# Kernel optimization log

Hardware: AMD Instinct MI355X
Metric: run time of the kernel (lower is better)

The kernel has to match this reference:

```python
import jax, jax.numpy as jnp
import numpy as np

# --- dims (match init_kwargs) ---
VOCAB = 16; D_MODEL = 512; NLAYERS = 4; LMAX = 1024; NCLASSES = 2
D_STATE = 128; D_CONV = 4; EXPAND = 2; HEADDIM = 64; PAD_IDX = 4
D_INNER = EXPAND * D_MODEL            # 1024
NHEADS = D_INNER // HEADDIM           # 16
CONV_DIM = D_INNER + 2 * D_STATE      # 1280 (ngroups=1)
D_IN_PROJ = 2 * D_INNER + 2 * D_STATE + NHEADS  # 2320
BATCH = 8; SEQ = 1024
EPS = 1e-5


def silu(x):
    return x * jax.nn.sigmoid(x)


def setup_inputs() -> dict:
    key = jax.random.key(0)
    ks = jax.random.split(key, 24)
    s = 0.02
    emb = jax.random.normal(ks[0], (VOCAB, D_MODEL), jnp.float32) * s
    emb = emb.at[PAD_IDX].set(0.0)  # padding_idx row is zero
    inp = {
        "tokens": jax.random.randint(ks[1], (BATCH, SEQ), 0, VOCAB),
        "attention_mask": jnp.ones((BATCH, SEQ), jnp.float32),
        "emb": emb,
        "pos_emb": jax.random.normal(ks[2], (1, LMAX, D_MODEL), jnp.float32) * s,
        "inp_w": jax.random.normal(ks[3], (D_MODEL, D_MODEL), jnp.float32) * s,
        "inp_b": jnp.zeros((D_MODEL,), jnp.float32),
        "ln_g": jnp.ones((D_MODEL,), jnp.float32),
        "ln_b": jnp.zeros((D_MODEL,), jnp.float32),
        # stacked per-layer Mamba2 params
        "in_proj_w": jax.random.normal(ks[4], (NLAYERS, D_IN_PROJ, D_MODEL), jnp.float32) * s,
        "conv_w": jax.random.normal(ks[5], (NLAYERS, CONV_DIM, D_CONV), jnp.float32) * 0.2,
        "conv_b": jnp.zeros((NLAYERS, CONV_DIM), jnp.float32),
        "dt_bias": jax.random.uniform(ks[6], (NLAYERS, NHEADS), jnp.float32, -4.0, -1.0),
        "A_log": jnp.log(jax.random.uniform(ks[7], (NLAYERS, NHEADS), jnp.float32, 1.0, 16.0)),
        "Dparam": jnp.ones((NLAYERS, NHEADS), jnp.float32),
        "norm_w": jnp.ones((NLAYERS, D_INNER), jnp.float32),
        "out_proj_w": jax.random.normal(ks[8], (NLAYERS, D_MODEL, D_INNER), jnp.float32) * s,
        "pooler_w": jax.random.normal(ks[9], (D_MODEL, D_MODEL), jnp.float32) * s,
        "pooler_b": jnp.zeros((D_MODEL,), jnp.float32),
        "cls_w1": jax.random.normal(ks[10], (D_MODEL // 2, D_MODEL), jnp.float32) * s,
        "cls_b1": jnp.zeros((D_MODEL // 2,), jnp.float32),
        "cls_w2": jax.random.normal(ks[11], (NCLASSES, D_MODEL // 2), jnp.float32) * s,
        "cls_b2": jnp.zeros((NCLASSES,), jnp.float32),
    }
    return inp


def mamba2_block(x, in_proj_w, conv_w, conv_b, dt_bias, A_log, Dp, norm_w, out_proj_w):
    """Mamba2 (ngroups=1, no proj biases, conv bias) on x:(B,L,d_model)."""
    Bsz, L, _ = x.shape
    zxbcdt = jnp.einsum("bld,ed->ble", x, in_proj_w)  # (B,L,2320)
    z = zxbcdt[..., :D_INNER]
    xBC = zxbcdt[..., D_INNER:D_INNER + CONV_DIM]
    dt = zxbcdt[..., D_INNER + CONV_DIM:]             # (B,L,H)
    # causal depthwise conv1d + silu
    xp = jnp.pad(xBC, ((0, 0), (D_CONV - 1, 0), (0, 0)))
    conv = conv_b
    for k in range(D_CONV):
        conv = conv + xp[:, k:k + L, :] * conv_w[:, k]
    xBC = silu(conv)
    xh = xBC[..., :D_INNER].reshape(Bsz, L, NHEADS, HEADDIM)
    Bc = xBC[..., D_INNER:D_INNER + D_STATE]          # (B,L,N)
    Cc = xBC[..., D_INNER + D_STATE:]                 # (B,L,N)
    dt = jax.nn.softplus(dt + dt_bias)                # (B,L,H)
    A = -jnp.exp(A_log)                               # (H,)
    dA = jnp.exp(dt * A)                              # (B,L,H)

    def step(h, inp):
        x_t, B_t, C_t, dt_t, dA_t = inp  # (B,H,P),(B,N),(B,N),(B,H),(B,H)
        h = h * dA_t[:, :, None, None] + (dt_t[:, :, None] * x_t)[..., None] * B_t[:, None, None, :]
        y = jnp.einsum("bhpn,bn->bhp", h, C_t)
        return h, y

    h0 = jnp.zeros((Bsz, NHEADS, HEADDIM, D_STATE), x.dtype)
    xs = (xh.transpose(1, 0, 2, 3), Bc.transpose(1, 0, 2), Cc.transpose(1, 0, 2),
          dt.transpose(1, 0, 2), dA.transpose(1, 0, 2))
    _, ys = jax.lax.scan(step, h0, xs)                # (L,B,H,P)
    y = ys.transpose(1, 0, 2, 3) + Dp[None, None, :, None] * xh
    y = y.reshape(Bsz, L, D_INNER)
    # gated RMSNorm: rmsnorm(y * silu(z)) * weight
    y = y * silu(z)
    y = y * jax.lax.rsqrt(jnp.mean(y * y, axis=-1, keepdims=True) + EPS) * norm_w
    return jnp.einsum("ble,de->bld", y, out_proj_w)


def reference(tokens, attention_mask, emb, pos_emb, inp_w, inp_b, ln_g, ln_b,
              in_proj_w, conv_w, conv_b, dt_bias, A_log, Dparam, norm_w, out_proj_w,
              pooler_w, pooler_b, cls_w1, cls_b1, cls_w2, cls_b2):
    L = tokens.shape[1]
    x = emb[tokens] + pos_emb[:, :L, :]
    # input_block: Linear -> LayerNorm (dropout is identity at eval)
    x = jnp.einsum("bld,ed->ble", x, inp_w) + inp_b
    mu = jnp.mean(x, -1, keepdims=True)
    var = jnp.mean((x - mu) ** 2, -1, keepdims=True)
    x = (x - mu) * jax.lax.rsqrt(var + EPS) * ln_g + ln_b
    x = x * attention_mask[..., None]
    for i in range(NLAYERS):
        res = x
        x = mamba2_block(x, in_proj_w[i], conv_w[i], conv_b[i], dt_bias[i],
                         A_log[i], Dparam[i], norm_w[i], out_proj_w[i])
        x = res + x
        x = x * attention_mask[..., None]
    pooled = (jnp.mean(x, axis=1) + jnp.max(x, axis=1)) * 0.5
    pooled = jax.nn.gelu(jnp.einsum("bd,ed->be", pooled, pooler_w) + pooler_b)
    h = jax.nn.gelu(jnp.einsum("bd,ed->be", pooled, cls_w1) + cls_b1)
    return jnp.einsum("bd,ed->be", h, cls_w2) + cls_b2
```

## Files before the change

kernel.cpp:

```cpp
#include <hip/hip_runtime.h>

#define EPS 1e-5f
typedef unsigned short u16;
typedef short s16x8 __attribute__((ext_vector_type(8)));
typedef float f32x4 __attribute__((ext_vector_type(4)));

__device__ __forceinline__ float siluf(float x) { return x / (1.0f + __expf(-x)); }
__device__ __forceinline__ float geluf(float x) {
    float u = 0.7978845608028654f * (x + 0.044715f * x * x * x);
    return 0.5f * x * (1.0f + tanhf(u));
}
__device__ __forceinline__ u16 f2bf(float f) {
    unsigned u = __float_as_uint(f);
    return (u16)((u + 0x7fffu + ((u >> 16) & 1u)) >> 16);
}
__device__ __forceinline__ float bf2f(u16 v) {
    return __uint_as_float(((unsigned)v) << 16);
}
struct u16x4 { u16 x, y, z, w; };
__device__ __forceinline__ u16x4 f2bf4(float4 v) {
    u16x4 r; r.x = f2bf(v.x); r.y = f2bf(v.y); r.z = f2bf(v.z); r.w = f2bf(v.w);
    return r;
}

#define GLOAD_LDS16(gp, lp) __builtin_amdgcn_global_load_lds( \
    (const __attribute__((address_space(1))) void*)(gp),      \
    (__attribute__((address_space(3))) void*)(lp), 16, 0, 0)

__global__ void k_cast_pad(const float* __restrict__ src, u16* __restrict__ dst) {
    int idx = blockIdx.x * 256 + threadIdx.x;
    if (idx >= 1245184) return;
    int e4 = idx * 4;
    int layer = e4 / 1245184;
    int rem   = e4 - layer * 1245184;
    int row   = rem >> 9;
    int k     = rem & 511;
    float4 v = make_float4(0.f, 0.f, 0.f, 0.f);
    if (row < 2320)
        v = *(const float4*)(src + (size_t)layer * 1187840 + (size_t)row * 512 + k);
    *(u16x4*)(dst + e4) = f2bf4(v);
}
__global__ void k_cast(const float* __restrict__ src, u16* __restrict__ dst, int n4) {
    int idx = blockIdx.x * 256 + threadIdx.x;
    if (idx >= n4) return;
    float4 v = *(const float4*)(src + (size_t)idx * 4);
    *(u16x4*)(dst + (size_t)idx * 4) = f2bf4(v);
}

__global__ void k_embed(const int* __restrict__ tok, const float* __restrict__ emb,
                        const float* __restrict__ pos, u16* __restrict__ out) {
    int idx = blockIdx.x * 256 + threadIdx.x;
    int d4 = idx & 127;
    int bl = idx >> 7;
    int l  = bl & 1023;
    float4 e = *(const float4*)(emb + tok[bl] * 512 + d4 * 4);
    float4 p = *(const float4*)(pos + l * 512 + d4 * 4);
    float4 v = make_float4(e.x + p.x, e.y + p.y, e.z + p.z, e.w + p.w);
    *(u16x4*)(out + (size_t)idx * 4) = f2bf4(v);
}

#define STAGE_I(buf, k0) do {                                                   \
    _Pragma("unroll")                                                           \
    for (int s_ = 0; s_ < 2; s_++) {                                            \
        int g_ = w * 2 + s_;                                                    \
        GLOAD_LDS16(A + (size_t)(m0 + g_ * 16 + lr) * 512 + (k0) + lk,          \
                    &Asm[buf][g_ * 512]);                                       \
    }                                                                           \
    GLOAD_LDS16(B + (size_t)(n0 + w * 16 + lr) * 512 + (k0) + lk,               \
                &Bsm[buf][w * 512]);                                            \
    } while (0)

#define COMPUTE_I(buf) do {                                                     \
    s16x8 af_[4], bf_[4];                                                       \
    _Pragma("unroll")                                                           \
    for (int i_ = 0; i_ < 4; i_++) {                                            \
        af_[i_] = *(const s16x8*)&Asm[buf][(wr * 4 + i_) * 512 + l * 8];        \
        bf_[i_] = *(const s16x8*)&Bsm[buf][(wc * 4 + i_) * 512 + l * 8];        \
    }                                                                           \
    _Pragma("unroll")                                                           \
    for (int i_ = 0; i_ < 4; i_++)                                              \
        _Pragma("unroll")                                                       \
        for (int j_ = 0; j_ < 4; j_++)                                          \
            acc[i_][j_] = __builtin_amdgcn_mfma_f32_16x16x32_bf16(              \
                af_[i_], bf_[j_], acc[i_][j_], 0, 0, 0);                        \
    } while (0)

__global__ __launch_bounds__(512, 4) void k_gemm_in(
    const u16* __restrict__ A, const u16* __restrict__ B,
    u16* __restrict__ zbf, u16* __restrict__ xbcbf, float* __restrict__ dtw) {
    __shared__ u16 Asm[3][8192];
    __shared__ u16 Bsm[3][4096];
    const int t = threadIdx.x;
    const int w = t >> 6, l = t & 63;
    const int wr = w >> 1, wc = w & 1;
    const int lr = l & 15, lk = (l >> 4) * 8;
    const int wgid = (blockIdx.x & 7) * 76 + (blockIdx.x >> 3);
    const int m0 = (wgid / 19) * 256;
    const int n0 = (wgid % 19) * 128;

    f32x4 acc[4][4] = {};

    STAGE_I(0, 0);
    STAGE_I(1, 32);
    for (int ki = 0; ki < 14; ki++) {
        asm volatile("s_waitcnt vmcnt(3)" ::: "memory");
        __builtin_amdgcn_s_barrier();
        STAGE_I((ki + 2) % 3, (ki + 2) * 32);
        COMPUTE_I(ki % 3);
    }
    asm volatile("s_waitcnt vmcnt(3)" ::: "memory");
    __builtin_amdgcn_s_barrier();
    COMPUTE_I(14 % 3);
    asm volatile("s_waitcnt vmcnt(0)" ::: "memory");
    __builtin_amdgcn_s_barrier();
    COMPUTE_I(15 % 3);

#pragma unroll
    for (int i = 0; i < 4; i++) {
        int mb = m0 + wr * 64 + i * 16 + (l >> 4) * 4;
#pragma unroll
        for (int j = 0; j < 4; j++) {
            int n = n0 + wc * 64 + j * 16 + (l & 15);
#pragma unroll
            for (int r2 = 0; r2 < 4; r2++) {
                int m = mb + r2;
                float v = acc[i][j][r2];
                if (n < 1024)      zbf[(size_t)m * 1024 + n] = f2bf(v);
                else if (n < 2304) xbcbf[(size_t)m * 1280 + (n - 1024)] = f2bf(v);
                else if (n < 2320) dtw[(size_t)m * 16 + (n - 2304)] = v;
            }
        }
    }
}

#define STAGE(buf, k0) do {                                                     \
    GLOAD_LDS16(A + (size_t)(m0 + w * 16 + lr) * K + (k0) + lk,                 \
                &Asm[buf][w * 512]);                                            \
    GLOAD_LDS16(B + (size_t)(n0 + w * 16 + lr) * K + (k0) + lk,                 \
                &Bsm[buf][w * 512]);                                            \
    } while (0)

#define COMPUTE(buf) do {                                                       \
    s16x8 af_[4], bf_[2];                                                       \
    _Pragma("unroll")                                                           \
    for (int i_ = 0; i_ < 4; i_++)                                              \
        af_[i_] = *(const s16x8*)&Asm[buf][(wr * 4 + i_) * 512 + l * 8];        \
    _Pragma("unroll")                                                           \
    for (int j_ = 0; j_ < 2; j_++)                                              \
        bf_[j_] = *(const s16x8*)&Bsm[buf][(wc * 2 + j_) * 512 + l * 8];        \
    _Pragma("unroll")                                                           \
    for (int i_ = 0; i_ < 4; i_++)                                              \
        _Pragma("unroll")                                                       \
        for (int j_ = 0; j_ < 2; j_++)                                          \
            acc[i_][j_] = __builtin_amdgcn_mfma_f32_16x16x32_bf16(              \
                af_[i_], bf_[j_], acc[i_][j_], 0, 0, 0);                        \
    } while (0)

template <int MODE>
__global__ __launch_bounds__(512) void k_gemm_mfma(
    const u16* __restrict__ A, const u16* __restrict__ B,
    const float* __restrict__ bias, float* __restrict__ C,
    u16* __restrict__ Cbf, const float* __restrict__ mask,
    int M, int N, int K, int gx) {
    __shared__ u16 Asm[3][4096];
    __shared__ u16 Bsm[3][4096];
    const int t = threadIdx.x;
    const int w = t >> 6, l = t & 63;
    const int wr = w >> 2, wc = w & 3;
    const int lr = l & 15, lk = (l >> 4) * 8;
    const int nwg = gridDim.x;
    const int q = nwg >> 3, r = nwg & 7;
    const int x8 = blockIdx.x & 7, d8 = blockIdx.x >> 3;
    const int wgid = (x8 < r) ? x8 * (q + 1) + d8 : r * (q + 1) + (x8 - r) * q + d8;
    const int m0 = (wgid / gx) * 128;
    const int n0 = (wgid % gx) * 128;

    f32x4 acc[4][2] = {};

    const int nk = K >> 5;
    STAGE(0, 0);
    STAGE(1, 32);
    for (int ki = 0; ki < nk - 2; ki++) {
        asm volatile("s_waitcnt vmcnt(2)" ::: "memory");
        __builtin_amdgcn_s_barrier();
        STAGE((ki + 2) % 3, (ki + 2) * 32);
        COMPUTE(ki % 3);
    }
    asm volatile("s_waitcnt vmcnt(2)" ::: "memory");
    __builtin_amdgcn_s_barrier();
    COMPUTE((nk - 2) % 3);
    asm volatile("s_waitcnt vmcnt(0)" ::: "memory");
    __builtin_amdgcn_s_barrier();
    COMPUTE((nk - 1) % 3);

#pragma unroll
    for (int i = 0; i < 4; i++) {
        int mb = m0 + wr * 64 + i * 16 + (l >> 4) * 4;
#pragma unroll
        for (int j = 0; j < 2; j++) {
            int n = n0 + wc * 32 + j * 16 + (l & 15);
#pragma unroll
            for (int r2 = 0; r2 < 4; r2++) {
                int m = mb + r2;
                float v = acc[i][j][r2];
                if (n < N) {
                    if (MODE == 1) v += bias[n];
                    size_t o = (size_t)m * N + n;
                    if (MODE == 2) {
                        v = (C[o] + v) * mask[m];
                        Cbf[o] = f2bf(v);
                    }
                    C[o] = v;
                }
            }
        }
    }
}

__global__ __launch_bounds__(128) void k_layernorm(
    float* __restrict__ x, const float* __restrict__ g,
    const float* __restrict__ b, const float* __restrict__ mask,
    u16* __restrict__ xbf) {
    __shared__ float2 sbuf[2];
    int bl = blockIdx.x;
    int t  = threadIdx.x;
    float4 v = *(float4*)(x + (size_t)bl * 512 + t * 4);
    float s = v.x + v.y + v.z + v.w;
    float q = v.x * v.x + v.y * v.y + v.z * v.z + v.w * v.w;
    for (int off = 32; off; off >>= 1) {
        s += __shfl_xor(s, off, 64);
        q += __shfl_xor(q, off, 64);
    }
    int wid = t >> 6, lane = t & 63;
    if (lane == 0) sbuf[wid] = make_float2(s, q);
    __syncthreads();
    float ts = sbuf[0].x + sbuf[1].x;
    float tq = sbuf[0].y + sbuf[1].y;
    float mu  = ts * (1.f / 512.f);
    float var = tq * (1.f / 512.f) - mu * mu;
    float inv = 1.0f / sqrtf(var + EPS);
    float mk  = mask[bl];
    float4 gg = *(const float4*)(g + t * 4);
    float4 bb = *(const float4*)(b + t * 4);
    float4 o;
    o.x = ((v.x - mu) * inv * gg.x + bb.x) * mk;
    o.y = ((v.y - mu) * inv * gg.y + bb.y) * mk;
    o.z = ((v.z - mu) * inv * gg.z + bb.z) * mk;
    o.w = ((v.w - mu) * inv * gg.w + bb.w) * mk;
    *(float4*)(x + (size_t)bl * 512 + t * 4) = o;
    *(u16x4*)(xbf + (size_t)bl * 512 + t * 4) = f2bf4(o);
}

__global__ __launch_bounds__(320) void k_conv(
    const u16* __restrict__ xbc_in, const float* __restrict__ cw,
    const float* __restrict__ cb, u16* __restrict__ xhbf,
    u16* __restrict__ bcbf) {
    int bid = blockIdx.x;
    int bl = (bid & 7) * 1024 + (bid >> 3);
    int l  = bl & 1023;
    int c  = threadIdx.x * 4;
    float4 w0 = *(const float4*)(cw + (c + 0) * 4);
    float4 w1 = *(const float4*)(cw + (c + 1) * 4);
    float4 w2 = *(const float4*)(cw + (c + 2) * 4);
    float4 w3 = *(const float4*)(cw + (c + 3) * 4);
    float4 a  = *(const float4*)(cb + c);
#pragma unroll
    for (int k = 0; k < 4; k++) {
        if (l + k - 3 >= 0) {
            u16x4 v = *(const u16x4*)(xbc_in + (size_t)(bl + k - 3) * 1280 + c);
            const float* wk0 = (const float*)&w0;
            const float* wk1 = (const float*)&w1;
            const float* wk2 = (const float*)&w2;
            const float* wk3 = (const float*)&w3;
            a.x = fmaf(bf2f(v.x), wk0[k], a.x);
            a.y = fmaf(bf2f(v.y), wk1[k], a.y);
            a.z = fmaf(bf2f(v.z), wk2[k], a.z);
            a.w = fmaf(bf2f(v.w), wk3[k], a.w);
        }
    }
    float4 o = make_float4(siluf(a.x), siluf(a.y), siluf(a.z), siluf(a.w));
    if (c < 1024)
        *(u16x4*)(xhbf + (size_t)bl * 1024 + c) = f2bf4(o);
    else
        *(u16x4*)(bcbf + (size_t)bl * 256 + (c - 1024)) = f2bf4(o);
}

__global__ __launch_bounds__(256) void k_ssd(
    const u16* __restrict__ xhbf, const u16* __restrict__ bcbf,
    const float* __restrict__ dt_raw, const float* __restrict__ dtbias,
    const float* __restrict__ alog, float* __restrict__ elbuf,
    float* __restrict__ y, float* __restrict__ scbuf) {
    int bid = blockIdx.x;
    int bhc = (bid & 7) * 128 + (bid >> 3);
    int c = bhc & 7, h = (bhc >> 3) & 15, b = bhc >> 7;
    const size_t row0 = (size_t)b * 1024 + c * 128;
    const int t = threadIdx.x, w = t >> 6, l = t & 63;
    const int wr = w >> 1, wc = w & 1;
    const int lr = l & 15, lk8 = (l >> 4) * 8;

    __shared__ float cl[128], dtl[128], wv[128];
    __shared__ float csh;
    __shared__ __align__(16) u16 shA[8704];
    __shared__ __align__(16) u16 shB[17408];

    float A = -__expf(alog[h]);
    float v = 0.f;
    if (t < 128) {
        float raw = dt_raw[(row0 + t) * 16 + h] + dtbias[h];
        float s = (raw > 20.f) ? raw : log1pf(__expf(raw));
        dtl[t] = s;
        v = s * A;
        int lane = t & 63;
#pragma unroll
        for (int off = 1; off < 64; off <<= 1) {
            float o = __shfl_up(v, off, 64);
            if (lane >= off) v += o;
        }
        if (t == 63) csh = v;
    }
    __syncthreads();
    if (t >= 64 && t < 128) v += csh;
    if (t < 128) {
        cl[t] = v;
        elbuf[(size_t)bhc * 128 + t] = __expf(v);
    }
    __syncthreads();
    if (t < 128) wv[t] = __expf(cl[127] - cl[t]);

    f32x4 acc[4][4] = {};
    for (int ks = 0; ks < 4; ks++) {
        int k0 = ks * 32;
#pragma unroll
        for (int s = 0; s < 2; s++) {
            int g = w * 2 + s;
            GLOAD_LDS16(bcbf + (row0 + g * 16 + lr) * 256 + 128 + k0 + lk8, &shA[g * 512]);
            GLOAD_LDS16(bcbf + (row0 + g * 16 + lr) * 256 +       k0 + lk8, &shA[4096 + g * 512]);
        }
        __syncthreads();
        s16x8 af[4], bfr[4];
#pragma unroll
        for (int i = 0; i < 4; i++) {
            af[i]  = *(const s16x8*)&shA[(wr * 4 + i) * 512 + l * 8];
            bfr[i] = *(const s16x8*)&shA[4096 + (wc * 4 + i) * 512 + l * 8];
        }
#pragma unroll
        for (int i = 0; i < 4; i++)
#pragma unroll
            for (int j = 0; j < 4; j++)
                acc[i][j] = __builtin_amdgcn_mfma_f32_16x16x32_bf16(af[i], bfr[j], acc[i][j], 0, 0, 0);
        __syncthreads();
    }

#pragma unroll
    for (int jj = 0; jj < 32; jj++) {
        int j = jj * 4 + w;
        float xv = bf2f(xhbf[(row0 + j) * 1024 + h * 64 + l]);
        shA[l * 136 + j] = f2bf(dtl[j] * xv);
    }
    __syncthreads();

    f32x4 acc2[4][2] = {};
    for (int half = 0; half < 2; half++) {
        if (wc == half) {
#pragma unroll
            for (int i = 0; i < 4; i++) {
#pragma unroll
                for (int j = 0; j < 4; j++) {
                    int col = half * 64 + j * 16 + (l & 15);
#pragma unroll
                    for (int r = 0; r < 4; r++) {
                        int row = wr * 64 + i * 16 + (l >> 4) * 4 + r;
                        float e = __expf(fminf(cl[row] - cl[col], 0.f));
                        float pv = (col <= row) ? acc[i][j][r] * e : 0.f;
                        shB[row * 72 + j * 16 + (l & 15)] = f2bf(pv);
                    }
                }
            }
        }
        __syncthreads();
#pragma unroll
        for (int ks = 0; ks < 2; ks++) {
            int kof = ks * 32;
            s16x8 pa[4], ub[2];
#pragma unroll
            for (int i = 0; i < 4; i++)
                pa[i] = *(const s16x8*)&shB[(wr * 64 + i * 16 + lr) * 72 + kof + lk8];
#pragma unroll
            for (int jj = 0; jj < 2; jj++)
                ub[jj] = *(const s16x8*)&shA[(wc * 32 + jj * 16 + lr) * 136 + half * 64 + kof + lk8];
#pragma unroll
            for (int i = 0; i < 4; i++)
#pragma unroll
                for (int jj = 0; jj < 2; jj++)
                    acc2[i][jj] = __builtin_amdgcn_mfma_f32_16x16x32_bf16(pa[i], ub[jj], acc2[i][jj], 0, 0, 0);
        }
        __syncthreads();
    }
#pragma unroll
    for (int i = 0; i < 4; i++)
#pragma unroll
        for (int jj = 0; jj < 2; jj++) {
            int p = wc * 32 + jj * 16 + (l & 15);
#pragma unroll
            for (int r = 0; r < 4; r++) {
                int row = wr * 64 + i * 16 + (l >> 4) * 4 + r;
                y[(row0 + row) * 1024 + h * 64 + p] = acc2[i][jj][r];
            }
        }

#pragma unroll
    for (int s = 0; s < 64; s++) {
        int j = s * 2 + (w & 1);
        int n = (w >> 1) * 64 + l;
        float bvv = bf2f(bcbf[(row0 + j) * 256 + n]);
        shB[n * 136 + j] = f2bf(wv[j] * bvv);
    }
    __syncthreads();

    f32x4 acc3[4][2] = {};
#pragma unroll
    for (int ks = 0; ks < 4; ks++) {
        int kof = ks * 32;
        s16x8 ua[4], bb[2];
#pragma unroll
        for (int i = 0; i < 4; i++)
            ua[i] = *(const s16x8*)&shA[(i * 16 + lr) * 136 + kof + lk8];
#pragma unroll
        for (int jj = 0; jj < 2; jj++)
            bb[jj] = *(const s16x8*)&shB[(w * 32 + jj * 16 + lr) * 136 + kof + lk8];
#pragma unroll
        for (int i = 0; i < 4; i++)
#pragma unroll
            for (int jj = 0; jj < 2; jj++)
                acc3[i][jj] = __builtin_amdgcn_mfma_f32_16x16x32_bf16(ua[i], bb[jj], acc3[i][jj], 0, 0, 0);
    }
#pragma unroll
    for (int i = 0; i < 4; i++)
#pragma unroll
        for (int jj = 0; jj < 2; jj++) {
            int n = w * 32 + jj * 16 + (l & 15);
#pragma unroll
            for (int r = 0; r < 4; r++) {
                int p = i * 16 + (l >> 4) * 4 + r;
                scbuf[(size_t)bhc * 8192 + (size_t)p * 128 + n] = acc3[i][jj][r];
            }
        }
}

__global__ __launch_bounds__(512) void k_states(float* __restrict__ scbuf,
                                                const float* __restrict__ elbuf) {
    int bh = blockIdx.x;
    int t = threadIdx.x;
    float4 h0 = {0, 0, 0, 0}, h1 = h0, h2 = h0, h3 = h0;
    size_t o = (size_t)t * 16;
    for (int c = 0; c < 8; c++) {
        int bhc = bh * 8 + c;
        float Tc = elbuf[(size_t)bhc * 128 + 127];
        float* p = scbuf + (size_t)bhc * 8192 + o;
        float4 s0 = *(float4*)(p + 0), s1 = *(float4*)(p + 4);
        float4 s2 = *(float4*)(p + 8), s3 = *(float4*)(p + 12);
        *(float4*)(p + 0) = h0; *(float4*)(p + 4) = h1;
        *(float4*)(p + 8) = h2; *(float4*)(p + 12) = h3;
        h0.x = fmaf(Tc, h0.x, s0.x); h0.y = fmaf(Tc, h0.y, s0.y);
        h0.z = fmaf(Tc, h0.z, s0.z); h0.w = fmaf(Tc, h0.w, s0.w);
        h1.x = fmaf(Tc, h1.x, s1.x); h1.y = fmaf(Tc, h1.y, s1.y);
        h1.z = fmaf(Tc, h1.z, s1.z); h1.w = fmaf(Tc, h1.w, s1.w);
        h2.x = fmaf(Tc, h2.x, s2.x); h2.y = fmaf(Tc, h2.y, s2.y);
        h2.z = fmaf(Tc, h2.z, s2.z); h2.w = fmaf(Tc, h2.w, s2.w);
        h3.x = fmaf(Tc, h3.x, s3.x); h3.y = fmaf(Tc, h3.y, s3.y);
        h3.z = fmaf(Tc, h3.z, s3.z); h3.w = fmaf(Tc, h3.w, s3.w);
    }
}

__global__ __launch_bounds__(256) void k_inter(
    const u16* __restrict__ xhbf, const u16* __restrict__ bcbf,
    const float* __restrict__ elbuf, const float* __restrict__ scbuf,
    const float* __restrict__ Dp, float* __restrict__ y) {
    int bid = blockIdx.x;
    int bhc = (bid & 7) * 128 + (bid >> 3);
    int c = bhc & 7, h = (bhc >> 3) & 15, b = bhc >> 7;
    const size_t row0 = (size_t)b * 1024 + c * 128;
    const int t = threadIdx.x, w = t >> 6, l = t & 63;
    const int wr = w >> 1, wc = w & 1;
    const int lr = l & 15, lk8 = (l >> 4) * 8;
    __shared__ __align__(16) u16 CStg[4096];
    __shared__ __align__(16) u16 HStg[2048];
    __shared__ float el[128];
    if (t < 128) el[t] = elbuf[(size_t)bhc * 128 + t];
    float Dv = Dp[h];

    f32x4 acc[4][2] = {};
    for (int ks = 0; ks < 4; ks++) {
        int k0 = ks * 32;
#pragma unroll
        for (int s = 0; s < 2; s++) {
            int g = w * 2 + s;
            GLOAD_LDS16(bcbf + (row0 + g * 16 + lr) * 256 + 128 + k0 + lk8, &CStg[g * 512]);
        }
        {
            int g = t >> 6, pr = (t >> 2) & 15, kq = t & 3;
            int p = g * 16 + pr;
            const float* src = scbuf + (size_t)bhc * 8192 + (size_t)p * 128 + k0 + kq * 8;
            float4 v0 = *(const float4*)src;
            float4 v1 = *(const float4*)(src + 4);
            s16x8 hv;
            hv[0] = (short)f2bf(v0.x); hv[1] = (short)f2bf(v0.y);
            hv[2] = (short)f2bf(v0.z); hv[3] = (short)f2bf(v0.w);
            hv[4] = (short)f2bf(v1.x); hv[5] = (short)f2bf(v1.y);
            hv[6] = (short)f2bf(v1.z); hv[7] = (short)f2bf(v1.w);
            *(s16x8*)&HStg[g * 512 + kq * 128 + pr * 8] = hv;
        }
        __syncthreads();
        s16x8 ca[4], hb[2];
#pragma unroll
        for (int i = 0; i < 4; i++)
            ca[i] = *(const s16x8*)&CStg[(wr * 4 + i) * 512 + l * 8];
#pragma unroll
        for (int jj = 0; jj < 2; jj++)
            hb[jj] = *(const s16x8*)&HStg[(wc * 2 + jj) * 512 + l * 8];
#pragma unroll
        for (int i = 0; i < 4; i++)
#pragma unroll
            for (int jj = 0; jj < 2; jj++)
                acc[i][jj] = __builtin_amdgcn_mfma_f32_16x16x32_bf16(ca[i], hb[jj], acc[i][jj], 0, 0, 0);
        __syncthreads();
    }
#pragma unroll
    for (int i = 0; i < 4; i++)
#pragma unroll
        for (int jj = 0; jj < 2; jj++) {
            int p = wc * 32 + jj * 16 + (l & 15);
#pragma unroll
            for (int r = 0; r < 4; r++) {
                int lrow = wr * 64 + i * 16 + (l >> 4) * 4 + r;
                size_t yo = (row0 + lrow) * 1024 + h * 64 + p;
                y[yo] += el[lrow] * acc[i][jj][r]
                       + Dv * bf2f(xhbf[(row0 + lrow) * 1024 + h * 64 + p]);
            }
        }
}

__global__ __launch_bounds__(256) void k_gate(
    const float* __restrict__ y, const u16* __restrict__ zbf,
    const float* __restrict__ nw, u16* __restrict__ ybf) {
    __shared__ float sbuf[4];
    int bl = blockIdx.x;
    int t  = threadIdx.x;
    float4 yv = *(const float4*)(y + (size_t)bl * 1024 + t * 4);
    u16x4 zv4 = *(const u16x4*)(zbf + (size_t)bl * 1024 + t * 4);
    float4 gv;
    gv.x = yv.x * siluf(bf2f(zv4.x));
    gv.y = yv.y * siluf(bf2f(zv4.y));
    gv.z = yv.z * siluf(bf2f(zv4.z));
    gv.w = yv.w * siluf(bf2f(zv4.w));
    float q = gv.x * gv.x + gv.y * gv.y + gv.z * gv.z + gv.w * gv.w;
    for (int off = 32; off; off >>= 1) q += __shfl_xor(q, off, 64);
    int wid = t >> 6, lane = t & 63;
    if (lane == 0) sbuf[wid] = q;
    __syncthreads();
    float tot = sbuf[0] + sbuf[1] + sbuf[2] + sbuf[3];
    float scale = 1.0f / sqrtf(tot * (1.f / 1024.f) + EPS);
    float4 nv = *(const float4*)(nw + t * 4);
    float4 o;
    o.x = gv.x * scale * nv.x;
    o.y = gv.y * scale * nv.y;
    o.z = gv.z * scale * nv.z;
    o.w = gv.w * scale * nv.w;
    *(u16x4*)(ybf + (size_t)bl * 1024 + t * 4) = f2bf4(o);
}

__global__ __launch_bounds__(256) void k_pool1(const float* __restrict__ x,
                                               float* __restrict__ psum,
                                               float* __restrict__ pmax) {
    int blk = blockIdx.x;
    int b = blk >> 6, lc = blk & 63;
    int t = threadIdx.x;
    const float* px = x + (size_t)b * 524288 + (size_t)lc * 16 * 512;
    float s0 = 0.f, s1 = 0.f, m0 = -3.0e38f, m1 = -3.0e38f;
#pragma unroll
    for (int r = 0; r < 16; r++) {
        float v0 = px[r * 512 + t];
        float v1 = px[r * 512 + t + 256];
        s0 += v0; s1 += v1;
        m0 = fmaxf(m0, v0); m1 = fmaxf(m1, v1);
    }
    psum[(size_t)blk * 512 + t]       = s0;
    psum[(size_t)blk * 512 + t + 256] = s1;
    pmax[(size_t)blk * 512 + t]       = m0;
    pmax[(size_t)blk * 512 + t + 256] = m1;
}

__global__ __launch_bounds__(256) void k_pool2(const float* __restrict__ psum,
                                               const float* __restrict__ pmax,
                                               float* __restrict__ pooled) {
    int idx = blockIdx.x * 256 + threadIdx.x;
    int b = idx >> 9, d = idx & 511;
    float s = 0.f, m = -3.0e38f;
    for (int c = 0; c < 64; c++) {
        s += psum[((size_t)b * 64 + c) * 512 + d];
        m = fmaxf(m, pmax[((size_t)b * 64 + c) * 512 + d]);
    }
    pooled[idx] = 0.5f * (s * (1.f / 1024.f) + m);
}

template <int ACT>
__global__ void k_fc(const float* __restrict__ in, const float* __restrict__ W,
                     const float* __restrict__ bias, float* __restrict__ out,
                     int BN, int N, int K) {
    int idx = blockIdx.x * 64 + threadIdx.x;
    if (idx >= BN) return;
    int b = idx / N, n = idx % N;
    const float* a = in + (size_t)b * K;
    const float* w = W + (size_t)n * K;
    float acc = 0.f;
    for (int k = 0; k < K; k += 4) {
        float4 av = *(const float4*)(a + k);
        float4 wv = *(const float4*)(w + k);
        acc += av.x * wv.x + av.y * wv.y + av.z * wv.z + av.w * wv.w;
    }
    float v = acc + bias[n];
    if (ACT == 1) v = geluf(v);
    out[idx] = v;
}

extern "C" void kernel_launch(void* const* d_in, const int* in_sizes, int n_in,
                              void* d_out, int out_size, void* d_ws, size_t ws_size,
                              hipStream_t stream) {
    (void)in_sizes; (void)n_in; (void)out_size; (void)ws_size;
    const int*   tok        = (const int*)  d_in[0];
    const float* mask       = (const float*)d_in[1];
    const float* emb        = (const float*)d_in[2];
    const float* pos        = (const float*)d_in[3];
    const float* inp_w      = (const float*)d_in[4];
    const float* inp_b      = (const float*)d_in[5];
    const float* ln_g       = (const float*)d_in[6];
    const float* ln_b       = (const float*)d_in[7];
    const float* in_proj_w  = (const float*)d_in[8];
    const float* conv_w     = (const float*)d_in[9];
    const float* conv_b     = (const float*)d_in[10];
    const float* dt_bias    = (const float*)d_in[11];
    const float* A_log      = (const float*)d_in[12];
    const float* Dparam     = (const float*)d_in[13];
    const float* norm_w     = (const float*)d_in[14];
    const float* out_proj_w = (const float*)d_in[15];
    const float* pooler_w   = (const float*)d_in[16];
    const float* pooler_b   = (const float*)d_in[17];
    const float* cls_w1     = (const float*)d_in[18];
    const float* cls_b1     = (const float*)d_in[19];
    const float* cls_w2     = (const float*)d_in[20];
    const float* cls_b2     = (const float*)d_in[21];
    float* out = (float*)d_out;

    float* ws     = (float*)d_ws;
    float* x      = ws;
    float* dt_raw = x + (size_t)8192 * 512;
    float* y      = dt_raw + (size_t)8192 * 16;
    float* elbuf  = y + (size_t)8192 * 1024;
    float* psum   = elbuf + 131072;
    float* pmax   = psum + 262144;
    float* pooled = pmax + 262144;
    float* pbuf   = pooled + 4096;
    float* cbuf   = pbuf + 4096;
    u16* x_bf    = (u16*)(cbuf + 2048);
    u16* z_bf    = x_bf + (size_t)8192 * 512;
    u16* xbc_in  = z_bf + (size_t)8192 * 1024;
    u16* y_bf    = xbc_in + (size_t)8192 * 1280;
    u16* xhbf    = y_bf + (size_t)8192 * 1024;
    u16* bcbf    = xhbf + (size_t)8192 * 1024;
    u16* wip_bf  = bcbf + (size_t)8192 * 256;
    u16* wop_bf  = wip_bf + (size_t)4 * 2432 * 512;
    u16* winp_bf = wop_bf + (size_t)4 * 512 * 1024;
    u16* xe_bf   = (u16*)y;
    float* scbuf = (float*)xbc_in;

    k_cast_pad<<<4864, 256, 0, stream>>>(in_proj_w, wip_bf);
    k_cast<<<2048, 256, 0, stream>>>(out_proj_w, wop_bf, 524288);
    k_cast<<<256, 256, 0, stream>>>(inp_w, winp_bf, 65536);

    k_embed<<<4096, 256, 0, stream>>>(tok, emb, pos, xe_bf);
    k_gemm_mfma<1><<<256, 512, 0, stream>>>(xe_bf, winp_bf, inp_b, x, nullptr,
                                            nullptr, 8192, 512, 512, 4);
    k_layernorm<<<8192, 128, 0, stream>>>(x, ln_g, ln_b, mask, x_bf);

    for (int i = 0; i < 4; i++) {
        k_gemm_in<<<608, 512, 0, stream>>>(x_bf, wip_bf + (size_t)i * 2432 * 512,
                                           z_bf, xbc_in, dt_raw);
        k_conv<<<8192, 320, 0, stream>>>(xbc_in, conv_w + (size_t)i * 1280 * 4,
                                         conv_b + (size_t)i * 1280, xhbf, bcbf);
        k_ssd<<<1024, 256, 0, stream>>>(xhbf, bcbf, dt_raw, dt_bias + i * 16,
                                        A_log + i * 16, elbuf, y, scbuf);
        k_states<<<128, 512, 0, stream>>>(scbuf, elbuf);
        k_inter<<<1024, 256, 0, stream>>>(xhbf, bcbf, elbuf, scbuf,
                                          Dparam + (size_t)i * 16, y);
        k_gate<<<8192, 256, 0, stream>>>(y, z_bf, norm_w + (size_t)i * 1024, y_bf);
        k_gemm_mfma<2><<<256, 512, 0, stream>>>(y_bf, wop_bf + (size_t)i * 512 * 1024,
                                                nullptr, x, x_bf, mask,
                                                8192, 512, 1024, 4);
    }

    k_pool1<<<512, 256, 0, stream>>>(x, psum, pmax);
    k_pool2<<<16, 256, 0, stream>>>(psum, pmax, pooled);
    k_fc<1><<<64, 64, 0, stream>>>(pooled, pooler_w, pooler_b, pbuf, 8 * 512, 512, 512);
    k_fc<1><<<32, 64, 0, stream>>>(pbuf, cls_w1, cls_b1, cbuf, 8 * 256, 256, 512);
    k_fc<0><<<1, 64, 0, stream>>>(cbuf, cls_w2, cls_b2, out, 8 * 2, 2, 256);
}
```

Before: 936.3 us.

## Store SSD intermediate y and chunk states in bf16, merge weight casts

The SSD intra-chunk output y and the per-chunk states are now stored as bf16 instead of fp32. This halves the memory traffic through k_ssd, k_states, k_inter and k_gate. k_inter can now stage the state tile straight into LDS with global_load_lds instead of converting it in registers. The three weight-cast launches are merged into one kernel. The cost is extra rounding: the y partial sums and the state recurrence inputs are rounded to bf16 between kernels, which lowers accuracy.

```diff
diff --git a/kernel.cpp b/kernel.cpp
--- a/kernel.cpp
+++ b/kernel.cpp
@@ -27,24 +27,29 @@
     (const __attribute__((address_space(1))) void*)(gp),      \
     (__attribute__((address_space(3))) void*)(lp), 16, 0, 0)
 
-__global__ void k_cast_pad(const float* __restrict__ src, u16* __restrict__ dst) {
+__global__ void k_casts(const float* __restrict__ ip, const float* __restrict__ op,
+                        const float* __restrict__ inp, u16* __restrict__ wip,
+                        u16* __restrict__ wop, u16* __restrict__ winp) {
     int idx = blockIdx.x * 256 + threadIdx.x;
-    if (idx >= 1245184) return;
-    int e4 = idx * 4;
-    int layer = e4 / 1245184;
-    int rem   = e4 - layer * 1245184;
-    int row   = rem >> 9;
-    int k     = rem & 511;
-    float4 v = make_float4(0.f, 0.f, 0.f, 0.f);
-    if (row < 2320)
-        v = *(const float4*)(src + (size_t)layer * 1187840 + (size_t)row * 512 + k);
-    *(u16x4*)(dst + e4) = f2bf4(v);
-}
-__global__ void k_cast(const float* __restrict__ src, u16* __restrict__ dst, int n4) {
-    int idx = blockIdx.x * 256 + threadIdx.x;
-    if (idx >= n4) return;
-    float4 v = *(const float4*)(src + (size_t)idx * 4);
-    *(u16x4*)(dst + (size_t)idx * 4) = f2bf4(v);
+    if (idx < 1245184) {
+        int e4 = idx * 4;
+        int layer = e4 / 1245184;
+        int rem   = e4 - layer * 1245184;
+        int row   = rem >> 9;
+        int k     = rem & 511;
+        float4 v = make_float4(0.f, 0.f, 0.f, 0.f);
+        if (row < 2320)
+            v = *(const float4*)(ip + (size_t)layer * 1187840 + (size_t)row * 512 + k);
+        *(u16x4*)(wip + e4) = f2bf4(v);
+    } else if (idx < 1245184 + 524288) {
+        int j = idx - 1245184;
+        float4 v = *(const float4*)(op + (size_t)j * 4);
+        *(u16x4*)(wop + (size_t)j * 4) = f2bf4(v);
+    } else if (idx < 1245184 + 524288 + 65536) {
+        int j = idx - 1245184 - 524288;
+        float4 v = *(const float4*)(inp + (size_t)j * 4);
+        *(u16x4*)(winp + (size_t)j * 4) = f2bf4(v);
+    }
 }
 
 __global__ void k_embed(const int* __restrict__ tok, const float* __restrict__ emb,
@@ -289,7 +294,7 @@
     const u16* __restrict__ xhbf, const u16* __restrict__ bcbf,
     const float* __restrict__ dt_raw, const float* __restrict__ dtbias,
     const float* __restrict__ alog, float* __restrict__ elbuf,
-    float* __restrict__ y, float* __restrict__ scbuf) {
+    u16* __restrict__ y16, u16* __restrict__ scb16) {
     int bid = blockIdx.x;
     int bhc = (bid & 7) * 128 + (bid >> 3);
     int c = bhc & 7, h = (bhc >> 3) & 15, b = bhc >> 7;
@@ -404,7 +409,7 @@
 #pragma unroll
             for (int r = 0; r < 4; r++) {
                 int row = wr * 64 + i * 16 + (l >> 4) * 4 + r;
-                y[(row0 + row) * 1024 + h * 64 + p] = acc2[i][jj][r];
+                y16[(row0 + row) * 1024 + h * 64 + p] = f2bf(acc2[i][jj][r]);
             }
         }
 
@@ -442,40 +447,45 @@
 #pragma unroll
             for (int r = 0; r < 4; r++) {
                 int p = i * 16 + (l >> 4) * 4 + r;
-                scbuf[(size_t)bhc * 8192 + (size_t)p * 128 + n] = acc3[i][jj][r];
+                scb16[(size_t)bhc * 8192 + (size_t)p * 128 + n] = f2bf(acc3[i][jj][r]);
             }
         }
 }
 
-__global__ __launch_bounds__(512) void k_states(float* __restrict__ scbuf,
+__global__ __launch_bounds__(512) void k_states(u16* __restrict__ scb16,
                                                 const float* __restrict__ elbuf) {
     int bh = blockIdx.x;
     int t = threadIdx.x;
-    float4 h0 = {0, 0, 0, 0}, h1 = h0, h2 = h0, h3 = h0;
+    float hreg[16];
+#pragma unroll
+    for (int j = 0; j < 16; j++) hreg[j] = 0.f;
     size_t o = (size_t)t * 16;
     for (int c = 0; c < 8; c++) {
         int bhc = bh * 8 + c;
         float Tc = elbuf[(size_t)bhc * 128 + 127];
-        float* p = scbuf + (size_t)bhc * 8192 + o;
-        float4 s0 = *(float4*)(p + 0), s1 = *(float4*)(p + 4);
-        float4 s2 = *(float4*)(p + 8), s3 = *(float4*)(p + 12);
-        *(float4*)(p + 0) = h0; *(float4*)(p + 4) = h1;
-        *(float4*)(p + 8) = h2; *(float4*)(p + 12) = h3;
-        h0.x = fmaf(Tc, h0.x, s0.x); h0.y = fmaf(Tc, h0.y, s0.y);
-        h0.z = fmaf(Tc, h0.z, s0.z); h0.w = fmaf(Tc, h0.w, s0.w);
-        h1.x = fmaf(Tc, h1.x, s1.x); h1.y = fmaf(Tc, h1.y, s1.y);
-        h1.z = fmaf(Tc, h1.z, s1.z); h1.w = fmaf(Tc, h1.w, s1.w);
-        h2.x = fmaf(Tc, h2.x, s2.x); h2.y = fmaf(Tc, h2.y, s2.y);
-        h2.z = fmaf(Tc, h2.z, s2.z); h2.w = fmaf(Tc, h2.w, s2.w);
-        h3.x = fmaf(Tc, h3.x, s3.x); h3.y = fmaf(Tc, h3.y, s3.y);
-        h3.z = fmaf(Tc, h3.z, s3.z); h3.w = fmaf(Tc, h3.w, s3.w);
+        u16* p = scb16 + (size_t)bhc * 8192 + o;
+        s16x8 v0 = *(s16x8*)(p);
+        s16x8 v1 = *(s16x8*)(p + 8);
+        s16x8 o0, o1;
+#pragma unroll
+        for (int j = 0; j < 8; j++) {
+            o0[j] = (short)f2bf(hreg[j]);
+            o1[j] = (short)f2bf(hreg[8 + j]);
+        }
+        *(s16x8*)(p)     = o0;
+        *(s16x8*)(p + 8) = o1;
+#pragma unroll
+        for (int j = 0; j < 8; j++) {
+            hreg[j]     = fmaf(Tc, hreg[j],     bf2f((u16)v0[j]));
+            hreg[8 + j] = fmaf(Tc, hreg[8 + j], bf2f((u16)v1[j]));
+        }
     }
 }
 
 __global__ __launch_bounds__(256) void k_inter(
     const u16* __restrict__ xhbf, const u16* __restrict__ bcbf,
-    const float* __restrict__ elbuf, const float* __restrict__ scbuf,
-    const float* __restrict__ Dp, float* __restrict__ y) {
+    const float* __restrict__ elbuf, const u16* __restrict__ scb16,
+    const float* __restrict__ Dp, u16* __restrict__ y16) {
     int bid = blockIdx.x;
     int bhc = (bid & 7) * 128 + (bid >> 3);
     int c = bhc & 7, h = (bhc >> 3) & 15, b = bhc >> 7;
@@ -497,19 +507,8 @@
             int g = w * 2 + s;
             GLOAD_LDS16(bcbf + (row0 + g * 16 + lr) * 256 + 128 + k0 + lk8, &CStg[g * 512]);
         }
-        {
-            int g = t >> 6, pr = (t >> 2) & 15, kq = t & 3;
-            int p = g * 16 + pr;
-            const float* src = scbuf + (size_t)bhc * 8192 + (size_t)p * 128 + k0 + kq * 8;
-            float4 v0 = *(const float4*)src;
-            float4 v1 = *(const float4*)(src + 4);
-            s16x8 hv;
-            hv[0] = (short)f2bf(v0.x); hv[1] = (short)f2bf(v0.y);
-            hv[2] = (short)f2bf(v0.z); hv[3] = (short)f2bf(v0.w);
-            hv[4] = (short)f2bf(v1.x); hv[5] = (short)f2bf(v1.y);
-            hv[6] = (short)f2bf(v1.z); hv[7] = (short)f2bf(v1.w);
-            *(s16x8*)&HStg[g * 512 + kq * 128 + pr * 8] = hv;
-        }
+        GLOAD_LDS16(scb16 + (size_t)bhc * 8192 + (size_t)(w * 16 + lr) * 128 + k0 + lk8,
+                    &HStg[w * 512]);
         __syncthreads();
         s16x8 ca[4], hb[2];
 #pragma unroll
@@ -534,25 +533,26 @@
             for (int r = 0; r < 4; r++) {
                 int lrow = wr * 64 + i * 16 + (l >> 4) * 4 + r;
                 size_t yo = (row0 + lrow) * 1024 + h * 64 + p;
-                y[yo] += el[lrow] * acc[i][jj][r]
-                       + Dv * bf2f(xhbf[(row0 + lrow) * 1024 + h * 64 + p]);
+                float yv = bf2f(y16[yo]) + el[lrow] * acc[i][jj][r]
+                         + Dv * bf2f(xhbf[(row0 + lrow) * 1024 + h * 64 + p]);
+                y16[yo] = f2bf(yv);
             }
         }
 }
 
 __global__ __launch_bounds__(256) void k_gate(
-    const float* __restrict__ y, const u16* __restrict__ zbf,
+    const u16* __restrict__ y16, const u16* __restrict__ zbf,
     const float* __restrict__ nw, u16* __restrict__ ybf) {
     __shared__ float sbuf[4];
     int bl = blockIdx.x;
     int t  = threadIdx.x;
-    float4 yv = *(const float4*)(y + (size_t)bl * 1024 + t * 4);
+    u16x4 yv4 = *(const u16x4*)(y16 + (size_t)bl * 1024 + t * 4);
     u16x4 zv4 = *(const u16x4*)(zbf + (size_t)bl * 1024 + t * 4);
     float4 gv;
-    gv.x = yv.x * siluf(bf2f(zv4.x));
-    gv.y = yv.y * siluf(bf2f(zv4.y));
-    gv.z = yv.z * siluf(bf2f(zv4.z));
-    gv.w = yv.w * siluf(bf2f(zv4.w));
+    gv.x = bf2f(yv4.x) * siluf(bf2f(zv4.x));
+    gv.y = bf2f(yv4.y) * siluf(bf2f(zv4.y));
+    gv.z = bf2f(yv4.z) * siluf(bf2f(zv4.z));
+    gv.w = bf2f(yv4.w) * siluf(bf2f(zv4.w));
     float q = gv.x * gv.x + gv.y * gv.y + gv.z * gv.z + gv.w * gv.w;
     for (int off = 32; off; off >>= 1) q += __shfl_xor(q, off, 64);
     int wid = t >> 6, lane = t & 63;
@@ -654,8 +654,7 @@
     float* ws     = (float*)d_ws;
     float* x      = ws;
     float* dt_raw = x + (size_t)8192 * 512;
-    float* y      = dt_raw + (size_t)8192 * 16;
-    float* elbuf  = y + (size_t)8192 * 1024;
+    float* elbuf  = dt_raw + (size_t)8192 * 16;
     float* psum   = elbuf + 131072;
     float* pmax   = psum + 262144;
     float* pooled = pmax + 262144;
@@ -667,15 +666,15 @@
     u16* y_bf    = xbc_in + (size_t)8192 * 1280;
     u16* xhbf    = y_bf + (size_t)8192 * 1024;
     u16* bcbf    = xhbf + (size_t)8192 * 1024;
-    u16* wip_bf  = bcbf + (size_t)8192 * 256;
+    u16* y16     = bcbf + (size_t)8192 * 256;
+    u16* wip_bf  = y16 + (size_t)8192 * 1024;
     u16* wop_bf  = wip_bf + (size_t)4 * 2432 * 512;
     u16* winp_bf = wop_bf + (size_t)4 * 512 * 1024;
-    u16* xe_bf   = (u16*)y;
-    float* scbuf = (float*)xbc_in;
-
-    k_cast_pad<<<4864, 256, 0, stream>>>(in_proj_w, wip_bf);
-    k_cast<<<2048, 256, 0, stream>>>(out_proj_w, wop_bf, 524288);
-    k_cast<<<256, 256, 0, stream>>>(inp_w, winp_bf, 65536);
+    u16* xe_bf   = (u16*)y16;
+    u16* scb16   = xbc_in;
+
+    k_casts<<<7168, 256, 0, stream>>>(in_proj_w, out_proj_w, inp_w,
+                                      wip_bf, wop_bf, winp_bf);
 
     k_embed<<<4096, 256, 0, stream>>>(tok, emb, pos, xe_bf);
     k_gemm_mfma<1><<<256, 512, 0, stream>>>(xe_bf, winp_bf, inp_b, x, nullptr,
@@ -688,11 +687,11 @@
         k_conv<<<8192, 320, 0, stream>>>(xbc_in, conv_w + (size_t)i * 1280 * 4,
                                          conv_b + (size_t)i * 1280, xhbf, bcbf);
         k_ssd<<<1024, 256, 0, stream>>>(xhbf, bcbf, dt_raw, dt_bias + i * 16,
-                                        A_log + i * 16, elbuf, y, scbuf);
-        k_states<<<128, 512, 0, stream>>>(scbuf, elbuf);
-        k_inter<<<1024, 256, 0, stream>>>(xhbf, bcbf, elbuf, scbuf,
-                                          Dparam + (size_t)i * 16, y);
-        k_gate<<<8192, 256, 0, stream>>>(y, z_bf, norm_w + (size_t)i * 1024, y_bf);
+                                        A_log + i * 16, elbuf, y16, scb16);
+        k_states<<<128, 512, 0, stream>>>(scb16, elbuf);
+        k_inter<<<1024, 256, 0, stream>>>(xhbf, bcbf, elbuf, scb16,
+                                          Dparam + (size_t)i * 16, y16);
+        k_gate<<<8192, 256, 0, stream>>>(y16, z_bf, norm_w + (size_t)i * 1024, y_bf);
         k_gemm_mfma<2><<<256, 512, 0, stream>>>(y_bf, wop_bf + (size_t)i * 512 * 1024,
                                                 nullptr, x, x_bf, mask,
                                                 8192, 512, 1024, 4);
```

Measured after the change: 899.6 us. 3.9% less time.
